# Performance work log

Measured on AMD Instinct MI355X. Metric: run time of the kernel, lower is better.

Reference implementation:

```python
import jax, jax.numpy as jnp
import numpy as np

B, F0, F1, E, C = 256, 39, 39, 16, 1  # batch, feature_nums[0], feature_nums[1], emb_size, w_channels
_ROWS, _COLS = np.tril_indices(F1, k=-1)  # strict lower triangle of (F1, F0); row-major order matches masked_select
I = _ROWS.shape[0]  # interaction_num = 741
BN_EPS = 1e-5


def setup_inputs() -> dict:
    key = jax.random.key(0)
    k1, k2, k3 = jax.random.split(key, 3)
    xi = jax.random.normal(k1, (B, F0, E), dtype=jnp.float32)
    xj = jax.random.normal(k2, (B, F1, E), dtype=jnp.float32)
    # W param is (1,1,C,E,E) in torch; keep the broadcastable core (C,E,E). Xavier-uniform bound.
    bound = float(np.sqrt(6.0 / (E + E)))
    W = jax.random.uniform(k3, (C, E, E), dtype=jnp.float32, minval=-bound, maxval=bound)
    gamma = jnp.ones((I,), dtype=jnp.float32)   # BatchNorm2d weight
    beta = jnp.zeros((I,), dtype=jnp.float32)   # BatchNorm2d bias
    return {"xi": xi, "xj": xj, "W": W, "gamma": gamma, "beta": beta}


def reference(xi, xj, W, gamma, beta):
    rows = jnp.asarray(_ROWS)
    cols = jnp.asarray(_COLS)
    # raw_cross[b,f1,f0,e1,e2] = xj[b,f1,e1] * xi[b,f0,e2]; only keep strict-lower-tri (f1,f0) pairs.
    # Compute triangular pairs directly instead of materializing the full (B,F1,F0,E,E) tensor.
    cross = xj[:, rows, :, None] * xi[:, cols, None, :]  # (B, I, E, E)
    # BatchNorm2d (training-mode batch stats, biased variance) over channels I
    mean = jnp.mean(cross, axis=(0, 2, 3), keepdims=True)            # (1, I, 1, 1)
    var = jnp.mean(jnp.square(cross - mean), axis=(0, 2, 3), keepdims=True)
    normed = (cross - mean) * jax.lax.rsqrt(var + BN_EPS)
    normed = normed * gamma[None, :, None, None] + beta[None, :, None, None]
    # broadcast multiply with W over w_channels, then transpose(1,2)
    out = normed[:, :, None, :, :] * W[None, None, :, :, :]          # (B, I, C, E, E)
    return jnp.transpose(out, (0, 2, 1, 3, 4))                        # (B, C, I, E, E)
```

## Files before the change

kernel.cpp:

```cpp
#include <hip/hip_runtime.h>
#include <math.h>

#define BB 256
#define FF 39
#define EE 16
#define II 741
#define BN_EPS 1e-5f

typedef float vfloat4 __attribute__((ext_vector_type(4)));


__global__ void rowsum_kernel(const float* __restrict__ xi,
                              const float* __restrict__ xj,
                              float* __restrict__ ws) {
    const int NROW = BB * FF;
    int t = blockIdx.x * blockDim.x + threadIdx.x;
    if (t >= 2 * NROW) return;
    int tensor = (t >= NROW) ? 1 : 0;
    int row = tensor ? (t - NROW) : t;
    const float* src = (tensor ? xj : xi) + row * EE;
    float s = 0.f, q = 0.f;
#pragma unroll
    for (int k = 0; k < 4; ++k) {
        vfloat4 v = reinterpret_cast<const vfloat4*>(src)[k];
        s += v.x + v.y + v.z + v.w;
        q += v.x * v.x + v.y * v.y + v.z * v.z + v.w * v.w;
    }
    float* base = ws + (tensor ? 2 * NROW : 0);
    base[row] = s;
    base[NROW + row] = q;
}

__global__ __launch_bounds__(256) void
stats_kernel(const float* __restrict__ gamma,
             const float* __restrict__ beta,
             float* __restrict__ ws) {
    int wid = (blockIdx.x * blockDim.x + threadIdx.x) >> 6;
    int lane = threadIdx.x & 63;
    if (wid >= II) return;
    int i = wid;
    int r = (int)((1.0f + sqrtf(8.0f * (float)i + 1.0f)) * 0.5f);
    while (r * (r - 1) / 2 > i) --r;
    while ((r + 1) * r / 2 <= i) ++r;
    int c = i - r * (r - 1) / 2;

    const int NROW = BB * FF;
    const float* Si = ws;
    const float* Qi = ws + NROW;
    const float* Sj = ws + 2 * NROW;
    const float* Qj = ws + 3 * NROW;

    float sumS = 0.f, sumQ = 0.f;
#pragma unroll
    for (int b = lane; b < BB; b += 64) {
        sumS += Sj[b * FF + r] * Si[b * FF + c];
        sumQ += Qj[b * FF + r] * Qi[b * FF + c];
    }
#pragma unroll
    for (int off = 32; off > 0; off >>= 1) {
        sumS += __shfl_xor(sumS, off);
        sumQ += __shfl_xor(sumQ, off);
    }
    if (lane == 0) {
        const float invN = 1.0f / (float)(BB * EE * EE);
        float mean = sumS * invN;
        float ex2 = sumQ * invN;
        float var = ex2 - mean * mean;
        float inv_std = 1.0f / sqrtf(var + BN_EPS);
        float a = gamma[i] * inv_std;
        float d = beta[i] - mean * a;
        vfloat4* T = reinterpret_cast<vfloat4*>(ws + 4 * NROW);
        vfloat4 e;
        e.x = a; e.y = d; e.z = (float)(r * EE); e.w = (float)(c * EE);
        T[i] = e;
    }
}

__global__ __launch_bounds__(256) void
cross_bn_kernel(const float* __restrict__ xi,
                const float* __restrict__ xj,
                const float* __restrict__ W,
                const float* __restrict__ ws,
                float* __restrict__ out) {
    const int NROW = BB * FF;
    const vfloat4* T = reinterpret_cast<const vfloat4*>(ws + 4 * NROW);

    int b = blockIdx.y;
    int t = threadIdx.x;
    int l = t & 63;
    int e1 = l >> 2;
    int e2q = l & 3;
    int wv = t >> 6;

    vfloat4 w4 = reinterpret_cast<const vfloat4*>(W)[e1 * 4 + e2q];

    const float* xib = xi + b * FF * EE;
    const float* xjb = xj + b * FF * EE;
    float* outb = out + (size_t)b * II * EE * EE;

    int ibase = blockIdx.x * 16 + wv * 4;
#pragma unroll
    for (int k = 0; k < 4; ++k) {
        int i = ibase + k;
        if (i >= II) break;
        vfloat4 tb = T[i];
        int joff = (int)tb.z;
        int coff = (int)tb.w;
        float xjs = xjb[joff + e1];
        vfloat4 xi4 = reinterpret_cast<const vfloat4*>(xib + coff)[e2q];
        vfloat4 o;
        o.x = (xjs * xi4.x * tb.x + tb.y) * w4.x;
        o.y = (xjs * xi4.y * tb.x + tb.y) * w4.y;
        o.z = (xjs * xi4.z * tb.x + tb.y) * w4.z;
        o.w = (xjs * xi4.w * tb.x + tb.y) * w4.w;
        vfloat4* dst = reinterpret_cast<vfloat4*>(outb + (size_t)i * (EE * EE)) + l;
        __builtin_nontemporal_store(o, dst);
    }
}

extern "C" void kernel_launch(void* const* d_in, const int* in_sizes, int n_in,
                              void* d_out, int out_size, void* d_ws, size_t ws_size,
                              hipStream_t stream) {
    const float* xi = (const float*)d_in[0];
    const float* xj = (const float*)d_in[1];
    const float* W = (const float*)d_in[2];
    const float* gamma = (const float*)d_in[3];
    const float* beta = (const float*)d_in[4];
    float* out = (float*)d_out;
    float* ws = (float*)d_ws;

    const int NROW = BB * FF;
    rowsum_kernel<<<dim3((2 * NROW + 255) / 256), 256, 0, stream>>>(xi, xj, ws);
    stats_kernel<<<dim3((II * 64 + 255) / 256), 256, 0, stream>>>(gamma, beta, ws);
    cross_bn_kernel<<<dim3((II + 15) / 16, BB), 256, 0, stream>>>(xi, xj, W, ws, out);
}
```

Baseline: 51.51 us.

## Fuse row-sum pass into stats kernel and batch more channels per wave

The separate row-sum kernel is removed. The stats kernel now recomputes per-row sums and squared sums directly from xi/xj for each channel, which saves one launch and a round trip through the workspace but repeats that work for every channel. The write kernel now handles 8 channels per wave instead of 4, issuing all table and input loads before the stores to expose more memory-level parallelism. It also launches fewer blocks, with a bounds-checked fallback for the tail.

```diff
diff --git a/kernel.cpp b/kernel.cpp
--- a/kernel.cpp
+++ b/kernel.cpp
@@ -10,29 +10,10 @@
 typedef float vfloat4 __attribute__((ext_vector_type(4)));
 
 
-__global__ void rowsum_kernel(const float* __restrict__ xi,
-                              const float* __restrict__ xj,
-                              float* __restrict__ ws) {
-    const int NROW = BB * FF;
-    int t = blockIdx.x * blockDim.x + threadIdx.x;
-    if (t >= 2 * NROW) return;
-    int tensor = (t >= NROW) ? 1 : 0;
-    int row = tensor ? (t - NROW) : t;
-    const float* src = (tensor ? xj : xi) + row * EE;
-    float s = 0.f, q = 0.f;
-#pragma unroll
-    for (int k = 0; k < 4; ++k) {
-        vfloat4 v = reinterpret_cast<const vfloat4*>(src)[k];
-        s += v.x + v.y + v.z + v.w;
-        q += v.x * v.x + v.y * v.y + v.z * v.z + v.w * v.w;
-    }
-    float* base = ws + (tensor ? 2 * NROW : 0);
-    base[row] = s;
-    base[NROW + row] = q;
-}
-
 __global__ __launch_bounds__(256) void
-stats_kernel(const float* __restrict__ gamma,
+stats_kernel(const float* __restrict__ xi,
+             const float* __restrict__ xj,
+             const float* __restrict__ gamma,
              const float* __restrict__ beta,
              float* __restrict__ ws) {
     int wid = (blockIdx.x * blockDim.x + threadIdx.x) >> 6;
@@ -44,17 +25,23 @@
     while ((r + 1) * r / 2 <= i) ++r;
     int c = i - r * (r - 1) / 2;
 
-    const int NROW = BB * FF;
-    const float* Si = ws;
-    const float* Qi = ws + NROW;
-    const float* Sj = ws + 2 * NROW;
-    const float* Qj = ws + 3 * NROW;
-
     float sumS = 0.f, sumQ = 0.f;
 #pragma unroll
     for (int b = lane; b < BB; b += 64) {
-        sumS += Sj[b * FF + r] * Si[b * FF + c];
-        sumQ += Qj[b * FF + r] * Qi[b * FF + c];
+        const vfloat4* xjr = reinterpret_cast<const vfloat4*>(xj + (b * FF + r) * EE);
+        const vfloat4* xic = reinterpret_cast<const vfloat4*>(xi + (b * FF + c) * EE);
+        float sj = 0.f, qj = 0.f, si = 0.f, qi = 0.f;
+#pragma unroll
+        for (int k = 0; k < 4; ++k) {
+            vfloat4 vj = xjr[k];
+            vfloat4 vi = xic[k];
+            sj += vj.x + vj.y + vj.z + vj.w;
+            qj += vj.x * vj.x + vj.y * vj.y + vj.z * vj.z + vj.w * vj.w;
+            si += vi.x + vi.y + vi.z + vi.w;
+            qi += vi.x * vi.x + vi.y * vi.y + vi.z * vi.z + vi.w * vi.w;
+        }
+        sumS += sj * si;
+        sumQ += qj * qi;
     }
 #pragma unroll
     for (int off = 32; off > 0; off >>= 1) {
@@ -69,21 +56,20 @@
         float inv_std = 1.0f / sqrtf(var + BN_EPS);
         float a = gamma[i] * inv_std;
         float d = beta[i] - mean * a;
-        vfloat4* T = reinterpret_cast<vfloat4*>(ws + 4 * NROW);
         vfloat4 e;
         e.x = a; e.y = d; e.z = (float)(r * EE); e.w = (float)(c * EE);
-        T[i] = e;
+        reinterpret_cast<vfloat4*>(ws)[i] = e;
     }
 }
 
+#define CPW 8
 __global__ __launch_bounds__(256) void
 cross_bn_kernel(const float* __restrict__ xi,
                 const float* __restrict__ xj,
                 const float* __restrict__ W,
                 const float* __restrict__ ws,
                 float* __restrict__ out) {
-    const int NROW = BB * FF;
-    const vfloat4* T = reinterpret_cast<const vfloat4*>(ws + 4 * NROW);
+    const vfloat4* T = reinterpret_cast<const vfloat4*>(ws);
 
     int b = blockIdx.y;
     int t = threadIdx.x;
@@ -98,23 +84,45 @@
     const float* xjb = xj + b * FF * EE;
     float* outb = out + (size_t)b * II * EE * EE;
 
-    int ibase = blockIdx.x * 16 + wv * 4;
+    int ibase = blockIdx.x * (4 * CPW) + wv * CPW;
+
+    if (ibase + CPW <= II) {
+        vfloat4 tb[CPW];
 #pragma unroll
-    for (int k = 0; k < 4; ++k) {
-        int i = ibase + k;
-        if (i >= II) break;
-        vfloat4 tb = T[i];
-        int joff = (int)tb.z;
-        int coff = (int)tb.w;
-        float xjs = xjb[joff + e1];
-        vfloat4 xi4 = reinterpret_cast<const vfloat4*>(xib + coff)[e2q];
-        vfloat4 o;
-        o.x = (xjs * xi4.x * tb.x + tb.y) * w4.x;
-        o.y = (xjs * xi4.y * tb.x + tb.y) * w4.y;
-        o.z = (xjs * xi4.z * tb.x + tb.y) * w4.z;
-        o.w = (xjs * xi4.w * tb.x + tb.y) * w4.w;
-        vfloat4* dst = reinterpret_cast<vfloat4*>(outb + (size_t)i * (EE * EE)) + l;
-        __builtin_nontemporal_store(o, dst);
+        for (int k = 0; k < CPW; ++k) tb[k] = T[ibase + k];
+        float xjs[CPW];
+        vfloat4 xi4[CPW];
+#pragma unroll
+        for (int k = 0; k < CPW; ++k) {
+            xjs[k] = xjb[(int)tb[k].z + e1];
+            xi4[k] = reinterpret_cast<const vfloat4*>(xib + (int)tb[k].w)[e2q];
+        }
+#pragma unroll
+        for (int k = 0; k < CPW; ++k) {
+            vfloat4 o;
+            o.x = (xjs[k] * xi4[k].x * tb[k].x + tb[k].y) * w4.x;
+            o.y = (xjs[k] * xi4[k].y * tb[k].x + tb[k].y) * w4.y;
+            o.z = (xjs[k] * xi4[k].z * tb[k].x + tb[k].y) * w4.z;
+            o.w = (xjs[k] * xi4[k].w * tb[k].x + tb[k].y) * w4.w;
+            vfloat4* dst = reinterpret_cast<vfloat4*>(outb + (size_t)(ibase + k) * (EE * EE)) + l;
+            __builtin_nontemporal_store(o, dst);
+        }
+    } else {
+#pragma unroll
+        for (int k = 0; k < CPW; ++k) {
+            int i = ibase + k;
+            if (i >= II) break;
+            vfloat4 tb = T[i];
+            float xjs = xjb[(int)tb.z + e1];
+            vfloat4 xi4 = reinterpret_cast<const vfloat4*>(xib + (int)tb.w)[e2q];
+            vfloat4 o;
+            o.x = (xjs * xi4.x * tb.x + tb.y) * w4.x;
+            o.y = (xjs * xi4.y * tb.x + tb.y) * w4.y;
+            o.z = (xjs * xi4.z * tb.x + tb.y) * w4.z;
+            o.w = (xjs * xi4.w * tb.x + tb.y) * w4.w;
+            vfloat4* dst = reinterpret_cast<vfloat4*>(outb + (size_t)i * (EE * EE)) + l;
+            __builtin_nontemporal_store(o, dst);
+        }
     }
 }
 
@@ -129,8 +137,7 @@
     float* out = (float*)d_out;
     float* ws = (float*)d_ws;
 
-    const int NROW = BB * FF;
-    rowsum_kernel<<<dim3((2 * NROW + 255) / 256), 256, 0, stream>>>(xi, xj, ws);
-    stats_kernel<<<dim3((II * 64 + 255) / 256), 256, 0, stream>>>(gamma, beta, ws);
-    cross_bn_kernel<<<dim3((II + 15) / 16, BB), 256, 0, stream>>>(xi, xj, W, ws, out);
+    stats_kernel<<<dim3((II * 64 + 255) / 256), 256, 0, stream>>>(xi, xj, gamma, beta, ws);
+    const int CPB = 4 * CPW;
+    cross_bn_kernel<<<dim3((II + CPB - 1) / CPB, BB), 256, 0, stream>>>(xi, xj, W, ws, out);
 }
```

After: 48.36 us. -6.1%, faster.
